# Kernel tuning notes

Measured on AMD Instinct MI355X. Metric: run time of the kernel, lower is better.

## Reference

```python
import math
import jax, jax.numpy as jnp
import numpy as np

HIDDEN = 768
NUM_HEADS = 12
HEAD_DIM = HIDDEN // NUM_HEADS
WINDOW = 256      # one-sided attention window
DILATION = 1
BATCH = 2
SEQ = 2048


def setup_inputs() -> dict:
    key = jax.random.key(0)
    ks = jax.random.split(key, 7)
    s = 1.0 / math.sqrt(HIDDEN)
    return {
        "hidden_states": jax.random.normal(ks[0], (BATCH, SEQ, HIDDEN), jnp.float32),
        "Wq": jax.random.normal(ks[1], (HIDDEN, HIDDEN), jnp.float32) * s,
        "bq": jnp.zeros((HIDDEN,), jnp.float32),
        "Wk": jax.random.normal(ks[2], (HIDDEN, HIDDEN), jnp.float32) * s,
        "bk": jnp.zeros((HIDDEN,), jnp.float32),
        "Wv": jax.random.normal(ks[3], (HIDDEN, HIDDEN), jnp.float32) * s,
        "bv": jnp.zeros((HIDDEN,), jnp.float32),
    }


def _band_mask(seq_len, dtype):
    # mask[i, j] = 1 iff |j - i| <= WINDOW * DILATION and (j - i) % DILATION == 0
    idx = jnp.arange(seq_len)
    rel = idx[None, :] - idx[:, None]  # [S, S]
    m = (jnp.abs(rel) <= WINDOW * DILATION) & (jnp.mod(rel, DILATION) == 0)
    return m.astype(dtype)


def reference(hidden_states, Wq, bq, Wk, bk, Wv, bv):
    B, S, M = hidden_states.shape
    H, D = NUM_HEADS, HEAD_DIM

    # torch nn.Linear: y = x @ W.T + b; query additionally scaled by 1/sqrt(head_dim)
    q = (hidden_states @ Wq.T + bq) / math.sqrt(D)
    k = hidden_states @ Wk.T + bk
    v = hidden_states @ Wv.T + bv

    # [B, S, M] -> [B, H, S, D]
    q = q.reshape(B, S, H, D).transpose(0, 2, 1, 3)
    k = k.reshape(B, S, H, D).transpose(0, 2, 1, 3)
    v = v.reshape(B, S, H, D).transpose(0, 2, 1, 3)

    # Dense scores, then MULTIPLICATIVE band mask (faithful: scores * mask, not additive -inf)
    scores = jnp.einsum("bhqd,bhkd->bhqk", q, k)
    mask = _band_mask(S, scores.dtype)  # [S, S], broadcasts over B, H
    scores = scores * mask

    probs = jax.nn.softmax(scores, axis=-1)  # [B, H, S, S]
    ctx = jnp.einsum("bhqk,bhkd->bhqd", probs, v)
    return ctx.transpose(0, 2, 1, 3).reshape(B, S, M)
```

## Files before the change

kernel.cpp:

```cpp
#include <hip/hip_runtime.h>
#include <hip/hip_bf16.h>
#include <cstdint>

#define SEQ    2048
#define HIDDEN 768
#define NHEAD  12
#define HDIM   64
#define WIN    256
#define BATCH  2
#define MTOT   (BATCH * SEQ)

typedef __attribute__((ext_vector_type(8))) short short8;
typedef __attribute__((ext_vector_type(4))) float f32x4;

union S8U4 { short8 s; uint4 u; };

__device__ __forceinline__ void bf16_split2(float a, float b, uint& h2, uint& l2) {
    union { __hip_bfloat162 v; uint u; } ch, cl;
    ch.v = __float22bfloat162_rn(make_float2(a, b));
    float af = __uint_as_float(ch.u << 16);
    float bf = __uint_as_float(ch.u & 0xFFFF0000u);
    cl.v = __float22bfloat162_rn(make_float2(a - af, b - bf));
    h2 = ch.u;
    l2 = cl.u;
}

__global__ __launch_bounds__(256) void proj_mfma_kernel(
    const float* __restrict__ X,
    const float* __restrict__ Wq, const float* __restrict__ bq,
    const float* __restrict__ Wk, const float* __restrict__ bk,
    const float* __restrict__ Wv, const float* __restrict__ bv,
    float* __restrict__ Qo, float* __restrict__ Ko, float* __restrict__ Vo)
{
    const int which = blockIdx.z;
    const float* __restrict__ W    = (which == 0) ? Wq : (which == 1) ? Wk : Wv;
    const float* __restrict__ bias = (which == 0) ? bq : (which == 1) ? bk : bv;
    float* __restrict__ out        = (which == 0) ? Qo : (which == 1) ? Ko : Vo;
    const float scale = (which == 0) ? 0.125f : 1.0f;

    __shared__ __align__(16) ushort Ahi[128 * 64];
    __shared__ __align__(16) ushort Alo[128 * 64];
    __shared__ __align__(16) ushort Bhi[64 * 64];
    __shared__ __align__(16) ushort Blo[64 * 64];

    const int t  = threadIdx.x;
    const int m0 = blockIdx.x * 128;
    const int h  = blockIdx.y;
    const int n0 = h * 64;

    const int w    = t >> 6;
    const int lane = t & 63;
    const int wr   = w >> 1;
    const int wc   = w & 1;
    const int lr   = lane & 15;
    const int lk   = lane >> 4;

    f32x4 acc[4][2];
#pragma unroll
    for (int i = 0; i < 4; ++i)
#pragma unroll
        for (int j = 0; j < 2; ++j) acc[i][j] = (f32x4){0.f, 0.f, 0.f, 0.f};

    for (int k0 = 0; k0 < HIDDEN; k0 += 64) {
        __syncthreads();
#pragma unroll
        for (int i = 0; i < 8; ++i) {
            int id  = t + i * 256;
            int row = id >> 4;
            int c4  = id & 15;
            const float4 xv = *(const float4*)&X[(size_t)(m0 + row) * HIDDEN + k0 + c4 * 4];
            uint h01, l01, h23, l23;
            bf16_split2(xv.x, xv.y, h01, l01);
            bf16_split2(xv.z, xv.w, h23, l23);
            int idx = (row * 64 + c4 * 4) ^ ((row & 7) << 3);
            *(uint2*)&Ahi[idx] = make_uint2(h01, h23);
            *(uint2*)&Alo[idx] = make_uint2(l01, l23);
        }
#pragma unroll
        for (int i = 0; i < 4; ++i) {
            int id  = t + i * 256;
            int row = id >> 4;
            int c4  = id & 15;
            const float4 wv4 = *(const float4*)&W[(size_t)(n0 + row) * HIDDEN + k0 + c4 * 4];
            uint h01, l01, h23, l23;
            bf16_split2(wv4.x, wv4.y, h01, l01);
            bf16_split2(wv4.z, wv4.w, h23, l23);
            int idx = (row * 64 + c4 * 4) ^ ((row & 7) << 3);
            *(uint2*)&Bhi[idx] = make_uint2(h01, h23);
            *(uint2*)&Blo[idx] = make_uint2(l01, l23);
        }
        __syncthreads();

#pragma unroll
        for (int s = 0; s < 2; ++s) {
            short8 ah[4], al[4], bh2[2], bl2[2];
#pragma unroll
            for (int fm = 0; fm < 4; ++fm) {
                int row = wr * 64 + fm * 16 + lr;
                int idx = (row * 64 + s * 32 + lk * 8) ^ ((row & 7) << 3);
                ah[fm] = *(const short8*)&Ahi[idx];
                al[fm] = *(const short8*)&Alo[idx];
            }
#pragma unroll
            for (int fn = 0; fn < 2; ++fn) {
                int row = wc * 32 + fn * 16 + lr;
                int idx = (row * 64 + s * 32 + lk * 8) ^ ((row & 7) << 3);
                bh2[fn] = *(const short8*)&Bhi[idx];
                bl2[fn] = *(const short8*)&Blo[idx];
            }
#pragma unroll
            for (int fm = 0; fm < 4; ++fm)
#pragma unroll
                for (int fn = 0; fn < 2; ++fn) {
                    acc[fm][fn] = __builtin_amdgcn_mfma_f32_16x16x32_bf16(
                        ah[fm], bh2[fn], acc[fm][fn], 0, 0, 0);
                    acc[fm][fn] = __builtin_amdgcn_mfma_f32_16x16x32_bf16(
                        ah[fm], bl2[fn], acc[fm][fn], 0, 0, 0);
                    acc[fm][fn] = __builtin_amdgcn_mfma_f32_16x16x32_bf16(
                        al[fm], bh2[fn], acc[fm][fn], 0, 0, 0);
                }
        }
    }

#pragma unroll
    for (int fn = 0; fn < 2; ++fn) {
        int d = wc * 32 + fn * 16 + lr;
        float bval = bias[n0 + d];
#pragma unroll
        for (int fm = 0; fm < 4; ++fm) {
#pragma unroll
            for (int r = 0; r < 4; ++r) {
                int m  = m0 + wr * 64 + fm * 16 + lk * 4 + r;
                int bb = m >> 11;
                int ss = m & (SEQ - 1);
                out[(((size_t)(bb * NHEAD + h) * SEQ) + ss) * HDIM + d] =
                    (acc[fm][fn][r] + bval) * scale;
            }
        }
    }
}

__global__ __launch_bounds__(256) void vprefix_kernel(
    const float* __restrict__ V, float* __restrict__ Vpre)
{
    const int bh    = blockIdx.x;
    const int d     = threadIdx.x & 63;
    const int chunk = threadIdx.x >> 6;
    const float* vb = &V[(size_t)bh * SEQ * HDIM];
    float* pb       = &Vpre[(size_t)bh * SEQ * HDIM];

    __shared__ float csum[4][64];
    const int s0 = chunk * 512;
    float sum = 0.f;
    for (int s = s0; s < s0 + 512; ++s) sum += vb[(size_t)s * HDIM + d];
    csum[chunk][d] = sum;
    __syncthreads();
    float run = 0.f;
    for (int c = 0; c < chunk; ++c) run += csum[c][d];
    for (int s = s0; s < s0 + 512; ++s) {
        run += vb[(size_t)s * HDIM + d];
        pb[(size_t)s * HDIM + d] = run;
    }
}

__global__ __launch_bounds__(512, 2) void attn_kernel(
    const float* __restrict__ Q, const float* __restrict__ K,
    const float* __restrict__ V, const float* __restrict__ Vpre,
    float* __restrict__ out)
{
    __shared__ __align__(16) ushort Khi[64 * 64], Klo[64 * 64];
    __shared__ __align__(16) ushort VThi[64 * 64], VTlo[64 * 64];
    __shared__ __align__(16) ushort Phi_s[8][16 * 64];
    __shared__ __align__(16) ushort Plo_s[8][16 * 64];

    const int t    = threadIdx.x;
    const int lane = t & 63;
    const int wv   = t >> 6;
    const int l15  = lane & 15;
    const int g2   = lane >> 4;

    const int L    = blockIdx.x;
    const int xcd  = L & 7;
    const int slot = L >> 3;
    const int bh   = xcd * 3 + (slot >> 4);
    const int qb   = slot & 15;
    const int b    = bh / NHEAD;
    const int h    = bh % NHEAD;
    const int i0   = qb * 128;
    const int i    = i0 + wv * 16 + l15;

    const float* kbase = &K[(size_t)bh * SEQ * HDIM];
    const float* vbase = &V[(size_t)bh * SEQ * HDIM];

    short8 qh[2], qlo[2];
    {
        const float* qrow = &Q[((size_t)bh * SEQ + i) * HDIM];
#pragma unroll
        for (int s = 0; s < 2; ++s) {
            float4 a = *(const float4*)&qrow[s * 32 + g2 * 8];
            float4 c = *(const float4*)&qrow[s * 32 + g2 * 8 + 4];
            S8U4 H, L;
            bf16_split2(a.x, a.y, H.u.x, L.u.x);
            bf16_split2(a.z, a.w, H.u.y, L.u.y);
            bf16_split2(c.x, c.y, H.u.z, L.u.z);
            bf16_split2(c.z, c.w, H.u.w, L.u.w);
            qh[s]  = H.s;
            qlo[s] = L.s;
        }
    }

    const int krow = t >> 3;
    const int kc   = (t & 7) * 8;
    const int vkp  = t >> 4;
    const int vdc  = (t & 15) * 4;
    float4 kpre[2], vp0, vp1;

    const int jlo_blk = max(0, i0 - WIN);
    const int jhi_blk = min(SEQ - 1, i0 + 127 + WIN);

    auto LOADT = [&](int jt2) {
        const float* kr = &kbase[(size_t)(jt2 + krow) * HDIM + kc];
        kpre[0] = *(const float4*)&kr[0];
        kpre[1] = *(const float4*)&kr[4];
        vp0 = *(const float4*)&vbase[(size_t)(jt2 + 2 * vkp) * HDIM + vdc];
        vp1 = *(const float4*)&vbase[(size_t)(jt2 + 2 * vkp + 1) * HDIM + vdc];
    };
    auto STORET = [&]() {
#pragma unroll
        for (int c = 0; c < 2; ++c) {
            uint h01, l01, h23, l23;
            bf16_split2(kpre[c].x, kpre[c].y, h01, l01);
            bf16_split2(kpre[c].z, kpre[c].w, h23, l23);
            int idx = (krow * 64 + kc + c * 4) ^ ((krow & 7) << 3);
            *(uint2*)&Khi[idx] = make_uint2(h01, h23);
            *(uint2*)&Klo[idx] = make_uint2(l01, l23);
        }
        float va[4] = {vp0.x, vp0.y, vp0.z, vp0.w};
        float vb4[4] = {vp1.x, vp1.y, vp1.z, vp1.w};
#pragma unroll
        for (int j = 0; j < 4; ++j) {
            int d = vdc + j;
            uint hj, lj;
            bf16_split2(va[j], vb4[j], hj, lj);
            int idx = (d * 64 + 2 * vkp) ^ ((d & 7) << 3);
            *(uint*)&VThi[idx] = hj;
            *(uint*)&VTlo[idx] = lj;
        }
    };

    float mrun = 0.f, lrun = 0.f;
    f32x4 ctx[4];
#pragma unroll
    for (int f = 0; f < 4; ++f) ctx[f] = (f32x4){0.f, 0.f, 0.f, 0.f};

    LOADT(jlo_blk);
    STORET();

    for (int jt = jlo_blk; jt <= jhi_blk; jt += 64) {
        const bool more = (jt + 64) <= jhi_blk;
        if (more) LOADT(jt + 64);
        __syncthreads();

        f32x4 sacc[4];
#pragma unroll
        for (int f = 0; f < 4; ++f) sacc[f] = (f32x4){0.f, 0.f, 0.f, 0.f};
#pragma unroll
        for (int s = 0; s < 2; ++s) {
            short8 kh[4], kl[4];
#pragma unroll
            for (int f = 0; f < 4; ++f) {
                int row = f * 16 + l15;
                int idx = (row * 64 + s * 32 + g2 * 8) ^ ((row & 7) << 3);
                kh[f] = *(const short8*)&Khi[idx];
                kl[f] = *(const short8*)&Klo[idx];
            }
#pragma unroll
            for (int f = 0; f < 4; ++f) {
                sacc[f] = __builtin_amdgcn_mfma_f32_16x16x32_bf16(kh[f], qh[s],  sacc[f], 0, 0, 0);
                sacc[f] = __builtin_amdgcn_mfma_f32_16x16x32_bf16(kh[f], qlo[s], sacc[f], 0, 0, 0);
                sacc[f] = __builtin_amdgcn_mfma_f32_16x16x32_bf16(kl[f], qh[s],  sacc[f], 0, 0, 0);
            }
        }

        float p[4][4];
        float tmax = -1e30f;
#pragma unroll
        for (int f = 0; f < 4; ++f)
#pragma unroll
            for (int r = 0; r < 4; ++r) {
                int j = jt + f * 16 + g2 * 4 + r;
                bool inw = (j >= i - WIN) && (j <= i + WIN);
                float sv_ = inw ? sacc[f][r] : -1e30f;
                p[f][r] = sv_;
                tmax = fmaxf(tmax, sv_);
            }
        tmax = fmaxf(tmax, __shfl_xor(tmax, 16));
        tmax = fmaxf(tmax, __shfl_xor(tmax, 32));
        float m_new = fmaxf(mrun, tmax);
        float resc  = __expf(mrun - m_new);
        float lsum  = 0.f;
#pragma unroll
        for (int f = 0; f < 4; ++f)
#pragma unroll
            for (int r = 0; r < 4; ++r) {
                float pe = __expf(p[f][r] - m_new);
                p[f][r] = pe;
                lsum += pe;
            }
        lsum += __shfl_xor(lsum, 16);
        lsum += __shfl_xor(lsum, 32);
        lrun = lrun * resc + lsum;
        mrun = m_new;
#pragma unroll
        for (int f = 0; f < 4; ++f) {
            ctx[f][0] *= resc; ctx[f][1] *= resc;
            ctx[f][2] *= resc; ctx[f][3] *= resc;
        }

#pragma unroll
        for (int f = 0; f < 4; ++f) {
            uint h01, l01, h23, l23;
            bf16_split2(p[f][0], p[f][1], h01, l01);
            bf16_split2(p[f][2], p[f][3], h23, l23);
            int idx = (l15 * 64 + f * 16 + g2 * 4) ^ ((l15 & 7) << 3);
            *(uint2*)&Phi_s[wv][idx] = make_uint2(h01, h23);
            *(uint2*)&Plo_s[wv][idx] = make_uint2(l01, l23);
        }

#pragma unroll
        for (int s = 0; s < 2; ++s) {
            int pidx = (l15 * 64 + s * 32 + g2 * 8) ^ ((l15 & 7) << 3);
            short8 ph = *(const short8*)&Phi_s[wv][pidx];
            short8 pl = *(const short8*)&Plo_s[wv][pidx];
#pragma unroll
            for (int f = 0; f < 4; ++f) {
                int row = f * 16 + l15;
                int idx = (row * 64 + s * 32 + g2 * 8) ^ ((row & 7) << 3);
                short8 vh = *(const short8*)&VThi[idx];
                short8 vl = *(const short8*)&VTlo[idx];
                ctx[f] = __builtin_amdgcn_mfma_f32_16x16x32_bf16(vh, ph, ctx[f], 0, 0, 0);
                ctx[f] = __builtin_amdgcn_mfma_f32_16x16x32_bf16(vl, ph, ctx[f], 0, 0, 0);
                ctx[f] = __builtin_amdgcn_mfma_f32_16x16x32_bf16(vh, pl, ctx[f], 0, 0, 0);
            }
        }

        __syncthreads();
        if (more) STORET();
    }

    const int jlo = max(0, i - WIN);
    const int jhi = min(SEQ - 1, i + WIN);
    const int cnt = jhi - jlo + 1;
    const float em   = __expf(-mrun);
    const float ltot = lrun + (float)(SEQ - cnt) * em;
    const float inv  = 1.f / ltot;

    const float* vpT = &Vpre[((size_t)bh * SEQ + (SEQ - 1)) * HDIM];
    const float* vpH = &Vpre[((size_t)bh * SEQ + jhi) * HDIM];
    const float* vpL = &Vpre[((size_t)bh * SEQ + (jlo - 1)) * HDIM];
    float* orow = &out[((size_t)(b * SEQ + i)) * HIDDEN + h * HDIM];

#pragma unroll
    for (int f = 0; f < 4; ++f) {
        int d0 = f * 16 + g2 * 4;
        float4 tt = *(const float4*)&vpT[d0];
        float4 hh = *(const float4*)&vpH[d0];
        float4 ll = {0.f, 0.f, 0.f, 0.f};
        if (jlo > 0) ll = *(const float4*)&vpL[d0];
        float4 o;
        o.x = (ctx[f][0] + em * (tt.x - hh.x + ll.x)) * inv;
        o.y = (ctx[f][1] + em * (tt.y - hh.y + ll.y)) * inv;
        o.z = (ctx[f][2] + em * (tt.z - hh.z + ll.z)) * inv;
        o.w = (ctx[f][3] + em * (tt.w - hh.w + ll.w)) * inv;
        *(float4*)&orow[d0] = o;
    }
}

extern "C" void kernel_launch(void* const* d_in, const int* in_sizes, int n_in,
                              void* d_out, int out_size, void* d_ws, size_t ws_size,
                              hipStream_t stream) {
    const float* X  = (const float*)d_in[0];
    const float* Wq = (const float*)d_in[1];
    const float* bq = (const float*)d_in[2];
    const float* Wk = (const float*)d_in[3];
    const float* bk = (const float*)d_in[4];
    const float* Wv = (const float*)d_in[5];
    const float* bv = (const float*)d_in[6];
    float* out = (float*)d_out;

    const size_t TEN = (size_t)BATCH * NHEAD * SEQ * HDIM;
    float* qf   = (float*)d_ws;
    float* kf   = qf + TEN;
    float* vf   = kf + TEN;
    float* vpre = vf + TEN;

    proj_mfma_kernel<<<dim3(MTOT / 128, NHEAD, 3), 256, 0, stream>>>(
        X, Wq, bq, Wk, bk, Wv, bv, qf, kf, vf);
    vprefix_kernel<<<dim3(BATCH * NHEAD), 256, 0, stream>>>(vf, vpre);
    attn_kernel<<<dim3((SEQ / 128) * BATCH * NHEAD), 512, 0, stream>>>(
        qf, kf, vf, vpre, out);
}
```

Measured before the change: 230.3 us.

## Prefetch next projection tile into registers and widen V prefix-sum parallelism

The projection GEMM now loads the next K-tile from global memory into registers before computing on the current shared-memory tile, then splits and stores it after a barrier. This is meant to hide global load latency behind the MFMA work. The V prefix-sum kernel moves from 256 to 1024 threads with 128-row chunks, so the serial scan per thread is shorter. The prefetch costs extra registers and an added barrier per iteration.

```diff
diff --git a/kernel.cpp b/kernel.cpp
--- a/kernel.cpp
+++ b/kernel.cpp
@@ -55,40 +55,58 @@
     const int lr   = lane & 15;
     const int lk   = lane >> 4;
 
-    f32x4 acc[4][2];
-#pragma unroll
-    for (int i = 0; i < 4; ++i)
-#pragma unroll
-        for (int j = 0; j < 2; ++j) acc[i][j] = (f32x4){0.f, 0.f, 0.f, 0.f};
-
-    for (int k0 = 0; k0 < HIDDEN; k0 += 64) {
-        __syncthreads();
+    const int srow = t >> 4;
+    const int sc4  = t & 15;
+
+    float4 a_f4[8], b_f4[4];
+
+    auto LOADT = [&](int k0) {
 #pragma unroll
         for (int i = 0; i < 8; ++i) {
-            int id  = t + i * 256;
-            int row = id >> 4;
-            int c4  = id & 15;
-            const float4 xv = *(const float4*)&X[(size_t)(m0 + row) * HIDDEN + k0 + c4 * 4];
+            int row = srow + i * 16;
+            a_f4[i] = *(const float4*)&X[(size_t)(m0 + row) * HIDDEN + k0 + sc4 * 4];
+        }
+#pragma unroll
+        for (int i = 0; i < 4; ++i) {
+            int row = srow + i * 16;
+            b_f4[i] = *(const float4*)&W[(size_t)(n0 + row) * HIDDEN + k0 + sc4 * 4];
+        }
+    };
+    auto STORET = [&]() {
+#pragma unroll
+        for (int i = 0; i < 8; ++i) {
+            int row = srow + i * 16;
             uint h01, l01, h23, l23;
-            bf16_split2(xv.x, xv.y, h01, l01);
-            bf16_split2(xv.z, xv.w, h23, l23);
-            int idx = (row * 64 + c4 * 4) ^ ((row & 7) << 3);
+            bf16_split2(a_f4[i].x, a_f4[i].y, h01, l01);
+            bf16_split2(a_f4[i].z, a_f4[i].w, h23, l23);
+            int idx = (row * 64 + sc4 * 4) ^ ((row & 7) << 3);
             *(uint2*)&Ahi[idx] = make_uint2(h01, h23);
             *(uint2*)&Alo[idx] = make_uint2(l01, l23);
         }
 #pragma unroll
         for (int i = 0; i < 4; ++i) {
-            int id  = t + i * 256;
-            int row = id >> 4;
-            int c4  = id & 15;
-            const float4 wv4 = *(const float4*)&W[(size_t)(n0 + row) * HIDDEN + k0 + c4 * 4];
+            int row = srow + i * 16;
             uint h01, l01, h23, l23;
-            bf16_split2(wv4.x, wv4.y, h01, l01);
-            bf16_split2(wv4.z, wv4.w, h23, l23);
-            int idx = (row * 64 + c4 * 4) ^ ((row & 7) << 3);
+            bf16_split2(b_f4[i].x, b_f4[i].y, h01, l01);
+            bf16_split2(b_f4[i].z, b_f4[i].w, h23, l23);
+            int idx = (row * 64 + sc4 * 4) ^ ((row & 7) << 3);
             *(uint2*)&Bhi[idx] = make_uint2(h01, h23);
             *(uint2*)&Blo[idx] = make_uint2(l01, l23);
         }
+    };
+
+    f32x4 acc[4][2];
+#pragma unroll
+    for (int i = 0; i < 4; ++i)
+#pragma unroll
+        for (int j = 0; j < 2; ++j) acc[i][j] = (f32x4){0.f, 0.f, 0.f, 0.f};
+
+    LOADT(0);
+    STORET();
+
+    for (int k0 = 0; k0 < HIDDEN; k0 += 64) {
+        const bool more = (k0 + 64) < HIDDEN;
+        if (more) LOADT(k0 + 64);
         __syncthreads();
 
 #pragma unroll
@@ -120,6 +138,9 @@
                         al[fm], bh2[fn], acc[fm][fn], 0, 0, 0);
                 }
         }
+
+        __syncthreads();
+        if (more) STORET();
     }
 
 #pragma unroll
@@ -140,7 +161,7 @@
     }
 }
 
-__global__ __launch_bounds__(256) void vprefix_kernel(
+__global__ __launch_bounds__(1024) void vprefix_kernel(
     const float* __restrict__ V, float* __restrict__ Vpre)
 {
     const int bh    = blockIdx.x;
@@ -149,15 +170,15 @@
     const float* vb = &V[(size_t)bh * SEQ * HDIM];
     float* pb       = &Vpre[(size_t)bh * SEQ * HDIM];
 
-    __shared__ float csum[4][64];
-    const int s0 = chunk * 512;
+    __shared__ float csum[16][64];
+    const int s0 = chunk * 128;
     float sum = 0.f;
-    for (int s = s0; s < s0 + 512; ++s) sum += vb[(size_t)s * HDIM + d];
+    for (int s = s0; s < s0 + 128; ++s) sum += vb[(size_t)s * HDIM + d];
     csum[chunk][d] = sum;
     __syncthreads();
     float run = 0.f;
     for (int c = 0; c < chunk; ++c) run += csum[c][d];
-    for (int s = s0; s < s0 + 512; ++s) {
+    for (int s = s0; s < s0 + 128; ++s) {
         run += vb[(size_t)s * HDIM + d];
         pb[(size_t)s * HDIM + d] = run;
     }
@@ -396,7 +417,7 @@
 
     proj_mfma_kernel<<<dim3(MTOT / 128, NHEAD, 3), 256, 0, stream>>>(
         X, Wq, bq, Wk, bk, Wv, bv, qf, kf, vf);
-    vprefix_kernel<<<dim3(BATCH * NHEAD), 256, 0, stream>>>(vf, vpre);
+    vprefix_kernel<<<dim3(BATCH * NHEAD), 1024, 0, stream>>>(vf, vpre);
     attn_kernel<<<dim3((SEQ / 128) * BATCH * NHEAD), 512, 0, stream>>>(
         qf, kf, vf, vpre, out);
 }
```

After: 280.1 us. 1.22x slower.
